# Kernel optimization log

Hardware: AMD Instinct MI355X
Metric: run time of the kernel (lower is better)

## Reference

```python
import jax, jax.numpy as jnp
import numpy as np

TOP_K = 2  # CompleteMOERTDETR default top_k


def setup_inputs() -> dict:
    key = jax.random.key(0)
    ks = jax.random.split(key, 6)
    B, S, D, E, Q, C = 128, 400, 256, 6, 300, 6
    return {
        "features": jax.random.normal(ks[0], (B, S, D), jnp.float32),            # flattened encoder feats
        "W1": jax.random.normal(ks[1], (D, D // 2), jnp.float32) * 0.02,          # Linear(input_dim, input_dim//2)
        "b1": jnp.zeros((D // 2,), jnp.float32),
        "W2": jax.random.normal(ks[2], (D // 2, E), jnp.float32) * 0.02,          # Linear(input_dim//2, num_experts)
        "b2": jnp.zeros((E,), jnp.float32),
        "expert_bboxes": jax.random.uniform(ks[3], (E, B, Q, 4), jnp.float32),    # per-expert pred_boxes
        "expert_class_scores": jax.random.normal(ks[4], (E, B, Q, C), jnp.float32),  # per-expert pred_logits
    }


def reference(features, W1, b1, W2, b2, expert_bboxes, expert_class_scores):
    # Router: Linear -> ReLU -> Linear -> Softmax  (router_net)
    h = jax.nn.relu(features @ W1 + b1)                    # [B,S,D/2]
    expert_logits = jax.nn.softmax(h @ W2 + b2, axis=-1)   # [B,S,E]
    # top-k gating over (already softmaxed) expert logits, then renormalizing softmax
    top_vals, top_idx = jax.lax.top_k(expert_logits, TOP_K)  # [B,S,K]
    routing_weights = jax.nn.softmax(top_vals, axis=-1)       # [B,S,K]

    S = features.shape[1]
    Q = expert_bboxes.shape[2]
    n = min(S, Q)  # combine loop runs over min(seq_len, actual_seq_len); static

    idx = top_idx[:, :n, :]           # [B,n,K]
    w = routing_weights[:, :n, :]     # [B,n,K]

    eb = jnp.transpose(expert_bboxes, (1, 2, 0, 3))        # [B,Q,E,4]
    ec = jnp.transpose(expert_class_scores, (1, 2, 0, 3))  # [B,Q,E,C]

    gb = jnp.take_along_axis(eb[:, :n], idx[..., None], axis=2)  # [B,n,K,4]
    gc = jnp.take_along_axis(ec[:, :n], idx[..., None], axis=2)  # [B,n,K,C]

    cb = jnp.einsum("bnkd,bnk->bnd", gb, w)  # weighted combine of bboxes
    cc = jnp.einsum("bnkc,bnk->bnc", gc, w)  # weighted combine of class scores

    # positions beyond n stay zero (combined_* initialized with zeros_like)
    combined_bboxes = jnp.zeros(eb.shape[:2] + (4,), eb.dtype).at[:, :n].set(cb)
    combined_class_scores = jnp.zeros(ec.shape[:2] + (ec.shape[-1],), ec.dtype).at[:, :n].set(cc)
    return combined_bboxes, combined_class_scores
```

## Files before the change

### kernel.cpp

```cpp
#include <hip/hip_runtime.h>
#include <math.h>

#define NB 128
#define SEQ 400
#define DIN 256
#define HID 128
#define NE 6
#define NQ 300
#define NC 6
#define NROW 300
#define M_TOTAL (NB*NROW)
#define ROWS_BLK 64
#define NBLK (M_TOTAL/ROWS_BLK)
#define KCHUNK 64
#define NCHUNK (DIN/KCHUNK)
#define TAU 5e-5f
#define OUT_BBOX_SZ (NB*NQ*4)
#define BM_WORDS (NBLK*2)
#define FIX_BLOCKS 128
#define FIX_GWAVES (FIX_BLOCKS*16)

#define WS_LO_OFF 65536
#define WS_BM_OFF 131072

using short8 = __attribute__((ext_vector_type(8))) short;
using f32x4  = __attribute__((ext_vector_type(4))) float;

__device__ inline unsigned short bf16_rne(float f) {
    unsigned int u = __float_as_uint(f);
    unsigned int r = (u + 0x7FFFu + ((u >> 16) & 1u)) >> 16;
    return (unsigned short)r;
}

__global__ __launch_bounds__(256)
void moe_prep(const float* __restrict__ W1, unsigned short* __restrict__ w1bf)
{
    int g = blockIdx.x * 256 + threadIdx.x;
    int frag = g >> 6;
    int lane = g & 63;
    int nf = frag & 1;
    int wv = (frag >> 1) & 3;
    int ks = (frag >> 3) & 1;
    int c  = frag >> 4;
    int n  = wv * 32 + nf * 16 + (lane & 15);
    int k0 = c * 64 + ks * 32 + (lane >> 4) * 8;

    short8 h8, l8;
    #pragma unroll
    for (int j = 0; j < 8; ++j) {
        float v = W1[(size_t)(k0 + j) * HID + n];
        unsigned short h = bf16_rne(v);
        h8[j] = (short)h;
        l8[j] = (short)bf16_rne(v - __uint_as_float((unsigned int)h << 16));
    }
    *(short8*)(w1bf + (size_t)frag * 512 + lane * 8)         = h8;
    *(short8*)(w1bf + 32768 + (size_t)frag * 512 + lane * 8) = l8;
}

__global__ __launch_bounds__(256)
void moe_main(const float* __restrict__ features, const float* __restrict__ b1,
              const unsigned short* __restrict__ w1bf, const float* __restrict__ W2,
              const float* __restrict__ b2, const float* __restrict__ ebox,
              const float* __restrict__ ecls, unsigned int* __restrict__ bitmap,
              float* __restrict__ out)
{
    __shared__ __align__(16) char s_raw[34048];
    __shared__ __align__(16) float s_w2[HID * NE];
    __shared__ unsigned int s_flagw[2];

    const int t    = (int)threadIdx.x;
    const int lane = t & 63;
    const int wv   = t >> 6;
    const int row0 = (int)blockIdx.x * ROWS_BLK;
    const int r15  = lane & 15;
    const int kq4  = lane >> 4;
    const char* w1b = (const char*)w1bf;

    if (t < 2) s_flagw[t] = 0u;
    for (int i = t; i < HID * NE; i += 256) s_w2[i] = W2[i];

    int  arow[4]; int akq[4]; long fbase[4];
    #pragma unroll
    for (int i = 0; i < 4; ++i) {
        int slot = i * 256 + t;
        int r  = slot >> 4;
        int kq = slot & 15;
        arow[i] = r; akq[i] = kq;
        int rowg = row0 + r;
        int bb = rowg / NROW;
        int ss = rowg - bb * NROW;
        fbase[i] = (long)(bb * SEQ + ss) * DIN;
    }

    f32x4 acc[4][2] = {};

    for (int c = 0; c < NCHUNK; ++c) {
        short8 bh[2][2], bl[2][2];
        #pragma unroll
        for (int ks = 0; ks < 2; ++ks)
            #pragma unroll
            for (int nf = 0; nf < 2; ++nf) {
                size_t base = (size_t)(c * 16 + ks * 8 + wv * 2 + nf) * 1024 + lane * 16;
                bh[ks][nf] = *(const short8*)(w1b + base);
                bl[ks][nf] = *(const short8*)(w1b + WS_LO_OFF + base);
            }
        __syncthreads();
        #pragma unroll
        for (int i = 0; i < 4; ++i) {
            float4 v = *(const float4*)(features + fbase[i] + c * KCHUNK + akq[i] * 4);
            unsigned short hx = bf16_rne(v.x), hy = bf16_rne(v.y),
                           hz = bf16_rne(v.z), hw = bf16_rne(v.w);
            float lxf = v.x - __uint_as_float((unsigned int)hx << 16);
            float lyf = v.y - __uint_as_float((unsigned int)hy << 16);
            float lzf = v.z - __uint_as_float((unsigned int)hz << 16);
            float lwf = v.w - __uint_as_float((unsigned int)hw << 16);
            short4 hi4 = make_short4((short)hx, (short)hy, (short)hz, (short)hw);
            short4 lo4 = make_short4((short)bf16_rne(lxf), (short)bf16_rne(lyf),
                                     (short)bf16_rne(lzf), (short)bf16_rne(lwf));
            int off = arow[i] * 128 + ((akq[i] * 8) ^ ((arow[i] & 7) << 4));
            *(short4*)(s_raw + off)        = hi4;
            *(short4*)(s_raw + 8192 + off) = lo4;
        }
        __syncthreads();

        #pragma unroll
        for (int ks = 0; ks < 2; ++ks) {
            const int kb = ks * 64 + kq4 * 16;
            #pragma unroll
            for (int mf = 0; mf < 4; ++mf) {
                int row  = mf * 16 + r15;
                int aoff = row * 128 + (kb ^ ((row & 7) << 4));
                short8 ah = *(const short8*)(s_raw + aoff);
                short8 al = *(const short8*)(s_raw + 8192 + aoff);
                #pragma unroll
                for (int nf = 0; nf < 2; ++nf) {
                    acc[mf][nf] = __builtin_amdgcn_mfma_f32_16x16x32_bf16(ah, bh[ks][nf], acc[mf][nf], 0, 0, 0);
                    acc[mf][nf] = __builtin_amdgcn_mfma_f32_16x16x32_bf16(al, bh[ks][nf], acc[mf][nf], 0, 0, 0);
                    acc[mf][nf] = __builtin_amdgcn_mfma_f32_16x16x32_bf16(ah, bl[ks][nf], acc[mf][nf], 0, 0, 0);
                }
            }
        }
    }

    __syncthreads();
    float* s_h = (float*)s_raw;
    #pragma unroll
    for (int nf = 0; nf < 2; ++nf) {
        int col = wv * 32 + nf * 16 + r15;
        float bias = b1[col];
        #pragma unroll
        for (int mf = 0; mf < 4; ++mf) {
            int row = mf * 16 + kq4 * 4;
            #pragma unroll
            for (int r = 0; r < 4; ++r)
                s_h[(row + r) * 132 + col] = fmaxf(acc[mf][nf][r] + bias, 0.f);
        }
    }
    __syncthreads();

    const int lrow = t >> 2;
    const int part = t & 3;
    float l[6] = {0.f, 0.f, 0.f, 0.f, 0.f, 0.f};
    {
        const float* hp = s_h + lrow * 132 + part * 32;
        const float* wp = s_w2 + part * 32 * NE;
        #pragma unroll
        for (int g = 0; g < 8; ++g) {
            float4 h4 = *(const float4*)(hp + g * 4);
            float w[24];
            #pragma unroll
            for (int q = 0; q < 6; ++q)
                *(float4*)(w + q * 4) = *(const float4*)(wp + g * 24 + q * 4);
            #pragma unroll
            for (int e = 0; e < 6; ++e)
                l[e] += h4.x * w[e] + h4.y * w[6 + e] + h4.z * w[12 + e] + h4.w * w[18 + e];
        }
    }
    #pragma unroll
    for (int e = 0; e < 6; ++e) { l[e] += __shfl_xor(l[e], 1); l[e] += __shfl_xor(l[e], 2); }

    if (part == 0) {
        float lg[NE];
        #pragma unroll
        for (int e = 0; e < NE; ++e) lg[e] = l[e] + b2[e];
        float m = lg[0];
        #pragma unroll
        for (int e = 1; e < NE; ++e) m = fmaxf(m, lg[e]);
        float p[NE]; float psum = 0.f;
        #pragma unroll
        for (int e = 0; e < NE; ++e) { p[e] = expf(lg[e] - m); psum += p[e]; }
        #pragma unroll
        for (int e = 0; e < NE; ++e) p[e] = p[e] / psum;

        int i0 = 0; float v0 = p[0];
        #pragma unroll
        for (int e = 1; e < NE; ++e) if (p[e] > v0) { v0 = p[e]; i0 = e; }
        int i1 = -1; float v1 = -1e38f;
        #pragma unroll
        for (int e = 0; e < NE; ++e) if (e != i0 && p[e] > v1) { v1 = p[e]; i1 = e; }
        float v2 = -1e38f;
        #pragma unroll
        for (int e = 0; e < NE; ++e) if (e != i0 && e != i1 && p[e] > v2) v2 = p[e];

        int rowg = row0 + lrow;
        bool flg = (v1 - v2 < TAU);
        if (flg) atomicOr(&s_flagw[lrow >> 5], 1u << (lrow & 31));

        if (!flg) {
            float e1 = expf(v1 - v0);
            float rw0 = 1.f / (1.f + e1);
            float rw1 = e1 / (1.f + e1);

            int bb = rowg / NROW;
            int ss = rowg - bb * NROW;
            size_t bo0 = ((size_t)(i0 * NB + bb) * NQ + ss) * 4;
            size_t bo1 = ((size_t)(i1 * NB + bb) * NQ + ss) * 4;
            float4 g0 = *(const float4*)(ebox + bo0);
            float4 g1 = *(const float4*)(ebox + bo1);
            float4 ob;
            ob.x = rw0 * g0.x + rw1 * g1.x;
            ob.y = rw0 * g0.y + rw1 * g1.y;
            ob.z = rw0 * g0.z + rw1 * g1.z;
            ob.w = rw0 * g0.w + rw1 * g1.w;
            *(float4*)(out + (size_t)rowg * 4) = ob;

            size_t co0 = ((size_t)(i0 * NB + bb) * NQ + ss) * NC;
            size_t co1 = ((size_t)(i1 * NB + bb) * NQ + ss) * NC;
            float* oc = out + OUT_BBOX_SZ + (size_t)rowg * NC;
            #pragma unroll
            for (int k = 0; k < NC; ++k)
                oc[k] = rw0 * ecls[co0 + k] + rw1 * ecls[co1 + k];
        }
    }

    __syncthreads();
    if (t == 0) {
        bitmap[(size_t)blockIdx.x * 2 + 0] = s_flagw[0];
        bitmap[(size_t)blockIdx.x * 2 + 1] = s_flagw[1];
    }
}

__global__ __launch_bounds__(1024)
void moe_fix(const float* __restrict__ features, const float* __restrict__ W1,
             const float* __restrict__ b1, const float* __restrict__ W2,
             const float* __restrict__ b2, const float* __restrict__ ebox,
             const float* __restrict__ ecls, const unsigned int* __restrict__ bitmap,
             float* __restrict__ out)
{
    __shared__ float s_w1[DIN * HID];
    __shared__ unsigned int s_bm[BM_WORDS];
    __shared__ int s_a[BM_WORDS];
    __shared__ int s_b[BM_WORDS];

    const int t    = (int)threadIdx.x;
    const int lane = t & 63;
    const int gw   = ((int)blockIdx.x << 4) + (t >> 6);

    {
        const float4* src = (const float4*)W1;
        float4* dst = (float4*)s_w1;
        #pragma unroll
        for (int i = 0; i < 8; ++i) dst[i * 1024 + t] = src[i * 1024 + t];
    }
    for (int i = t; i < BM_WORDS; i += 1024) {
        unsigned int w = bitmap[i];
        s_bm[i] = w;
        s_a[i] = (int)__popc(w);
    }
    __syncthreads();

    int* src = s_a; int* dst = s_b;
    for (int s = 1; s < BM_WORDS; s <<= 1) {
        for (int i = t; i < BM_WORDS; i += 1024)
            dst[i] = src[i] + (i >= s ? src[i - s] : 0);
        __syncthreads();
        int* tmp = src; src = dst; dst = tmp;
    }
    const int N = src[BM_WORDS - 1];

    const int c0 = lane * 2;

    for (int o = gw; o < N; o += FIX_GWAVES) {
        int lo = 0, hi = BM_WORDS - 1;
        while (lo < hi) {
            int mid = (lo + hi) >> 1;
            if (src[mid] > o) hi = mid; else lo = mid + 1;
        }
        int excl = lo ? src[lo - 1] : 0;
        int k = o - excl;
        unsigned int w = s_bm[lo];
        for (int j = 0; j < k; ++j) w &= w - 1;
        int row = lo * 32 + (int)__builtin_ctz(w);

        int bb = row / NROW;
        int ss = row - bb * NROW;
        const float* fp = features + (size_t)(bb * SEQ + ss) * DIN;

        float a0 = 0.f, a1 = 0.f;
        #pragma unroll 8
        for (int d = 0; d < DIN; d += 4) {
            float4 f4 = *(const float4*)(fp + d);
            float2 w0 = *(const float2*)(s_w1 + (d + 0) * HID + c0);
            float2 w1 = *(const float2*)(s_w1 + (d + 1) * HID + c0);
            float2 w2 = *(const float2*)(s_w1 + (d + 2) * HID + c0);
            float2 w3 = *(const float2*)(s_w1 + (d + 3) * HID + c0);
            a0 = fmaf(f4.x, w0.x, a0); a1 = fmaf(f4.x, w0.y, a1);
            a0 = fmaf(f4.y, w1.x, a0); a1 = fmaf(f4.y, w1.y, a1);
            a0 = fmaf(f4.z, w2.x, a0); a1 = fmaf(f4.z, w2.y, a1);
            a0 = fmaf(f4.w, w3.x, a0); a1 = fmaf(f4.w, w3.y, a1);
        }
        float h0 = fmaxf(a0 + b1[c0], 0.f);
        float h1 = fmaxf(a1 + b1[c0 + 1], 0.f);

        float lg[NE];
        #pragma unroll
        for (int e = 0; e < NE; ++e) {
            float v = h0 * W2[c0 * NE + e] + h1 * W2[(c0 + 1) * NE + e];
            #pragma unroll
            for (int off = 1; off < 64; off <<= 1) v += __shfl_xor(v, off);
            lg[e] = v + b2[e];
        }
        float mx = lg[0];
        #pragma unroll
        for (int e = 1; e < NE; ++e) mx = fmaxf(mx, lg[e]);
        float pr[NE]; float psum = 0.f;
        #pragma unroll
        for (int e = 0; e < NE; ++e) { pr[e] = expf(lg[e] - mx); psum += pr[e]; }
        #pragma unroll
        for (int e = 0; e < NE; ++e) pr[e] = pr[e] / psum;

        int i0 = 0; float v0 = pr[0];
        #pragma unroll
        for (int e = 1; e < NE; ++e) if (pr[e] > v0) { v0 = pr[e]; i0 = e; }
        int i1 = -1; float v1 = -1e38f;
        #pragma unroll
        for (int e = 0; e < NE; ++e) if (e != i0 && pr[e] > v1) { v1 = pr[e]; i1 = e; }

        if (lane == 0) {
            float e1 = expf(v1 - v0);
            float rw0 = 1.f / (1.f + e1);
            float rw1 = e1 / (1.f + e1);
            size_t bo0 = ((size_t)(i0 * NB + bb) * NQ + ss) * 4;
            size_t bo1 = ((size_t)(i1 * NB + bb) * NQ + ss) * 4;
            float4 g0 = *(const float4*)(ebox + bo0);
            float4 g1 = *(const float4*)(ebox + bo1);
            float4 ob;
            ob.x = rw0 * g0.x + rw1 * g1.x;
            ob.y = rw0 * g0.y + rw1 * g1.y;
            ob.z = rw0 * g0.z + rw1 * g1.z;
            ob.w = rw0 * g0.w + rw1 * g1.w;
            *(float4*)(out + (size_t)row * 4) = ob;
            size_t co0 = ((size_t)(i0 * NB + bb) * NQ + ss) * NC;
            size_t co1 = ((size_t)(i1 * NB + bb) * NQ + ss) * NC;
            float* oc = out + OUT_BBOX_SZ + (size_t)row * NC;
            #pragma unroll
            for (int kk = 0; kk < NC; ++kk)
                oc[kk] = rw0 * ecls[co0 + kk] + rw1 * ecls[co1 + kk];
        }
    }
}

extern "C" void kernel_launch(void* const* d_in, const int* in_sizes, int n_in,
                              void* d_out, int out_size, void* d_ws, size_t ws_size,
                              hipStream_t stream)
{
    const float* features = (const float*)d_in[0];
    const float* W1   = (const float*)d_in[1];
    const float* b1   = (const float*)d_in[2];
    const float* W2   = (const float*)d_in[3];
    const float* b2   = (const float*)d_in[4];
    const float* ebox = (const float*)d_in[5];
    const float* ecls = (const float*)d_in[6];
    float* out = (float*)d_out;

    unsigned short* w1bf   = (unsigned short*)d_ws;
    unsigned int*   bitmap = (unsigned int*)((char*)d_ws + WS_BM_OFF);

    hipLaunchKernelGGL(moe_prep, dim3(16), dim3(256), 0, stream, W1, w1bf);
    hipLaunchKernelGGL(moe_main, dim3(NBLK), dim3(256), 0, stream,
                       features, b1, w1bf, W2, b2, ebox, ecls, bitmap, out);
    hipLaunchKernelGGL(moe_fix, dim3(FIX_BLOCKS), dim3(1024), 0, stream,
                       features, W1, b1, W2, b2, ebox, ecls, bitmap, out);
}
```

Baseline: 44.16 us.

## Launch one wavefront per row in fix kernel with early bitmap exit

The fallback kernel used to run 128 blocks of 1024 threads. Each block copied all of W1 (128 KB) into LDS and built a prefix-sum scan over the flag bitmap to compact the flagged rows. It now launches one 64-thread block per row (38400 blocks). Each block checks its bitmap bit and returns at once if the row is not flagged, reading W1 from global memory or cache. This removes the per-block LDS staging and scan cost. In exchange it pays launch and scheduling overhead for tens of thousands of mostly empty blocks.

```diff
diff --git a/kernel.cpp b/kernel.cpp
--- a/kernel.cpp
+++ b/kernel.cpp
@@ -16,9 +16,6 @@
 #define NCHUNK (DIN/KCHUNK)
 #define TAU 5e-5f
 #define OUT_BBOX_SZ (NB*NQ*4)
-#define BM_WORDS (NBLK*2)
-#define FIX_BLOCKS 128
-#define FIX_GWAVES (FIX_BLOCKS*16)
 
 #define WS_LO_OFF 65536
 #define WS_BM_OFF 131072
@@ -240,123 +237,83 @@
     }
 }
 
-__global__ __launch_bounds__(1024)
+__global__ __launch_bounds__(64)
 void moe_fix(const float* __restrict__ features, const float* __restrict__ W1,
              const float* __restrict__ b1, const float* __restrict__ W2,
              const float* __restrict__ b2, const float* __restrict__ ebox,
              const float* __restrict__ ecls, const unsigned int* __restrict__ bitmap,
              float* __restrict__ out)
 {
-    __shared__ float s_w1[DIN * HID];
-    __shared__ unsigned int s_bm[BM_WORDS];
-    __shared__ int s_a[BM_WORDS];
-    __shared__ int s_b[BM_WORDS];
-
-    const int t    = (int)threadIdx.x;
-    const int lane = t & 63;
-    const int gw   = ((int)blockIdx.x << 4) + (t >> 6);
-
-    {
-        const float4* src = (const float4*)W1;
-        float4* dst = (float4*)s_w1;
-        #pragma unroll
-        for (int i = 0; i < 8; ++i) dst[i * 1024 + t] = src[i * 1024 + t];
-    }
-    for (int i = t; i < BM_WORDS; i += 1024) {
-        unsigned int w = bitmap[i];
-        s_bm[i] = w;
-        s_a[i] = (int)__popc(w);
-    }
-    __syncthreads();
-
-    int* src = s_a; int* dst = s_b;
-    for (int s = 1; s < BM_WORDS; s <<= 1) {
-        for (int i = t; i < BM_WORDS; i += 1024)
-            dst[i] = src[i] + (i >= s ? src[i - s] : 0);
-        __syncthreads();
-        int* tmp = src; src = dst; dst = tmp;
-    }
-    const int N = src[BM_WORDS - 1];
-
+    const int row = (int)blockIdx.x;
+    if (!((bitmap[row >> 5] >> (row & 31)) & 1u)) return;
+
+    const int lane = (int)threadIdx.x;
     const int c0 = lane * 2;
 
-    for (int o = gw; o < N; o += FIX_GWAVES) {
-        int lo = 0, hi = BM_WORDS - 1;
-        while (lo < hi) {
-            int mid = (lo + hi) >> 1;
-            if (src[mid] > o) hi = mid; else lo = mid + 1;
-        }
-        int excl = lo ? src[lo - 1] : 0;
-        int k = o - excl;
-        unsigned int w = s_bm[lo];
-        for (int j = 0; j < k; ++j) w &= w - 1;
-        int row = lo * 32 + (int)__builtin_ctz(w);
-
-        int bb = row / NROW;
-        int ss = row - bb * NROW;
-        const float* fp = features + (size_t)(bb * SEQ + ss) * DIN;
-
-        float a0 = 0.f, a1 = 0.f;
-        #pragma unroll 8
-        for (int d = 0; d < DIN; d += 4) {
-            float4 f4 = *(const float4*)(fp + d);
-            float2 w0 = *(const float2*)(s_w1 + (d + 0) * HID + c0);
-            float2 w1 = *(const float2*)(s_w1 + (d + 1) * HID + c0);
-            float2 w2 = *(const float2*)(s_w1 + (d + 2) * HID + c0);
-            float2 w3 = *(const float2*)(s_w1 + (d + 3) * HID + c0);
-            a0 = fmaf(f4.x, w0.x, a0); a1 = fmaf(f4.x, w0.y, a1);
-            a0 = fmaf(f4.y, w1.x, a0); a1 = fmaf(f4.y, w1.y, a1);
-            a0 = fmaf(f4.z, w2.x, a0); a1 = fmaf(f4.z, w2.y, a1);
-            a0 = fmaf(f4.w, w3.x, a0); a1 = fmaf(f4.w, w3.y, a1);
-        }
-        float h0 = fmaxf(a0 + b1[c0], 0.f);
-        float h1 = fmaxf(a1 + b1[c0 + 1], 0.f);
-
-        float lg[NE];
-        #pragma unroll
-        for (int e = 0; e < NE; ++e) {
-            float v = h0 * W2[c0 * NE + e] + h1 * W2[(c0 + 1) * NE + e];
-            #pragma unroll
-            for (int off = 1; off < 64; off <<= 1) v += __shfl_xor(v, off);
-            lg[e] = v + b2[e];
-        }
-        float mx = lg[0];
-        #pragma unroll
-        for (int e = 1; e < NE; ++e) mx = fmaxf(mx, lg[e]);
-        float pr[NE]; float psum = 0.f;
-        #pragma unroll
-        for (int e = 0; e < NE; ++e) { pr[e] = expf(lg[e] - mx); psum += pr[e]; }
-        #pragma unroll
-        for (int e = 0; e < NE; ++e) pr[e] = pr[e] / psum;
-
-        int i0 = 0; float v0 = pr[0];
-        #pragma unroll
-        for (int e = 1; e < NE; ++e) if (pr[e] > v0) { v0 = pr[e]; i0 = e; }
-        int i1 = -1; float v1 = -1e38f;
-        #pragma unroll
-        for (int e = 0; e < NE; ++e) if (e != i0 && pr[e] > v1) { v1 = pr[e]; i1 = e; }
-
-        if (lane == 0) {
-            float e1 = expf(v1 - v0);
-            float rw0 = 1.f / (1.f + e1);
-            float rw1 = e1 / (1.f + e1);
-            size_t bo0 = ((size_t)(i0 * NB + bb) * NQ + ss) * 4;
-            size_t bo1 = ((size_t)(i1 * NB + bb) * NQ + ss) * 4;
-            float4 g0 = *(const float4*)(ebox + bo0);
-            float4 g1 = *(const float4*)(ebox + bo1);
-            float4 ob;
-            ob.x = rw0 * g0.x + rw1 * g1.x;
-            ob.y = rw0 * g0.y + rw1 * g1.y;
-            ob.z = rw0 * g0.z + rw1 * g1.z;
-            ob.w = rw0 * g0.w + rw1 * g1.w;
-            *(float4*)(out + (size_t)row * 4) = ob;
-            size_t co0 = ((size_t)(i0 * NB + bb) * NQ + ss) * NC;
-            size_t co1 = ((size_t)(i1 * NB + bb) * NQ + ss) * NC;
-            float* oc = out + OUT_BBOX_SZ + (size_t)row * NC;
-            #pragma unroll
-            for (int kk = 0; kk < NC; ++kk)
-                oc[kk] = rw0 * ecls[co0 + kk] + rw1 * ecls[co1 + kk];
-        }
+    int bb = row / NROW;
+    int ss = row - bb * NROW;
+    const float* fp = features + (size_t)(bb * SEQ + ss) * DIN;
+
+    float a0 = 0.f, a1 = 0.f;
+    #pragma unroll 8
+    for (int d = 0; d < DIN; d += 4) {
+        float4 f4 = *(const float4*)(fp + d);
+        float2 w0 = *(const float2*)(W1 + (size_t)(d + 0) * HID + c0);
+        float2 w1 = *(const float2*)(W1 + (size_t)(d + 1) * HID + c0);
+        float2 w2 = *(const float2*)(W1 + (size_t)(d + 2) * HID + c0);
+        float2 w3 = *(const float2*)(W1 + (size_t)(d + 3) * HID + c0);
+        a0 = fmaf(f4.x, w0.x, a0); a1 = fmaf(f4.x, w0.y, a1);
+        a0 = fmaf(f4.y, w1.x, a0); a1 = fmaf(f4.y, w1.y, a1);
+        a0 = fmaf(f4.z, w2.x, a0); a1 = fmaf(f4.z, w2.y, a1);
+        a0 = fmaf(f4.w, w3.x, a0); a1 = fmaf(f4.w, w3.y, a1);
+    }
+    float h0 = fmaxf(a0 + b1[c0], 0.f);
+    float h1 = fmaxf(a1 + b1[c0 + 1], 0.f);
+
+    float lg[NE];
+    #pragma unroll
+    for (int e = 0; e < NE; ++e) {
+        float v = h0 * W2[c0 * NE + e] + h1 * W2[(c0 + 1) * NE + e];
+        #pragma unroll
+        for (int off = 1; off < 64; off <<= 1) v += __shfl_xor(v, off);
+        lg[e] = v + b2[e];
+    }
+    float mx = lg[0];
+    #pragma unroll
+    for (int e = 1; e < NE; ++e) mx = fmaxf(mx, lg[e]);
+    float pr[NE]; float psum = 0.f;
+    #pragma unroll
+    for (int e = 0; e < NE; ++e) { pr[e] = expf(lg[e] - mx); psum += pr[e]; }
+    #pragma unroll
+    for (int e = 0; e < NE; ++e) pr[e] = pr[e] / psum;
+
+    int i0 = 0; float v0 = pr[0];
+    #pragma unroll
+    for (int e = 1; e < NE; ++e) if (pr[e] > v0) { v0 = pr[e]; i0 = e; }
+    int i1 = -1; float v1 = -1e38f;
+    #pragma unroll
+    for (int e = 0; e < NE; ++e) if (e != i0 && pr[e] > v1) { v1 = pr[e]; i1 = e; }
+
+    if (lane == 0) {
+        float e1 = expf(v1 - v0);
+        float rw0 = 1.f / (1.f + e1);
+        float rw1 = e1 / (1.f + e1);
+        size_t bo0 = ((size_t)(i0 * NB + bb) * NQ + ss) * 4;
+        size_t bo1 = ((size_t)(i1 * NB + bb) * NQ + ss) * 4;
+        float4 g0 = *(const float4*)(ebox + bo0);
+        float4 g1 = *(const float4*)(ebox + bo1);
+        float4 ob;
+        ob.x = rw0 * g0.x + rw1 * g1.x;
+        ob.y = rw0 * g0.y + rw1 * g1.y;
+        ob.z = rw0 * g0.z + rw1 * g1.z;
+        ob.w = rw0 * g0.w + rw1 * g1.w;
+        *(float4*)(out + (size_t)row * 4) = ob;
+        size_t co0 = ((size_t)(i0 * NB + bb) * NQ + ss) * NC;
+        size_t co1 = ((size_t)(i1 * NB + bb) * NQ + ss) * NC;
+        float* oc = out + OUT_BBOX_SZ + (size_t)row * NC;
+        #pragma unroll
+        for (int kk = 0; kk < NC; ++kk)
+            oc[kk] = rw0 * ecls[co0 + kk] + rw1 * ecls[co1 + kk];
     }
 }
 
@@ -379,6 +336,6 @@
     hipLaunchKernelGGL(moe_prep, dim3(16), dim3(256), 0, stream, W1, w1bf);
     hipLaunchKernelGGL(moe_main, dim3(NBLK), dim3(256), 0, stream,
                        features, b1, w1bf, W2, b2, ebox, ecls, bitmap, out);
-    hipLaunchKernelGGL(moe_fix, dim3(FIX_BLOCKS), dim3(1024), 0, stream,
+    hipLaunchKernelGGL(moe_fix, dim3(M_TOTAL), dim3(64), 0, stream,
                        features, W1, b1, W2, b2, ebox, ecls, bitmap, out);
 }
```

After: 46.06 us. +4.3%, slower.
